# Performance work log

Measured on AMD Instinct MI355X. Metric: run time of the kernel, lower is better.

Reference implementation:

```python
import jax, jax.numpy as jnp
import numpy as np

SUBSET_CHANNELS = 128


def setup_inputs() -> dict:
    key = jax.random.key(0)
    k_in, k_q, k_k, k_v = jax.random.split(key, 4)
    B, S, C, D = 8, 2048, 1024, SUBSET_CHANNELS
    scale = 1.0 / np.sqrt(C)  # ~ default torch Linear init scale
    return {
        "input": jax.random.normal(k_in, (B, S, C), dtype=jnp.float32),
        "Wq": jax.random.normal(k_q, (C, D), dtype=jnp.float32) * scale,
        "Wk": jax.random.normal(k_k, (C, D), dtype=jnp.float32) * scale,
        "Wv": jax.random.normal(k_v, (C, D), dtype=jnp.float32) * scale,
    }


def reference(input, Wq, Wk, Wv):
    # Projections (bias=False): [B,S,C] @ [C,D] -> [B,S,D]
    Q = input @ Wq
    K = input @ Wk
    V = input @ Wv
    D = Wq.shape[1]
    # scores[b, i, j] = Q[b,i,:] . K[b,j,:], scaled by sqrt(subset_channels)
    scores = jnp.einsum("bqd,bkd->bqk", Q, K) / jnp.sqrt(jnp.asarray(D, Q.dtype))
    # NOTE: original applies softmax over dim=1 (the QUERY axis), non-standard.
    att = jax.nn.softmax(scores, axis=1)
    # output[b, i, :] = sum_j att[b,i,j] * V[b,j,:]
    return jnp.einsum("bqk,bkd->bqd", att, V)
```

## Files before the change

kernel.cpp:

```cpp
#include <hip/hip_runtime.h>
#include <hip/hip_bf16.h>

typedef __bf16 bf16_t;
typedef bf16_t bf16x4 __attribute__((ext_vector_type(4)));
typedef bf16_t bf16x8 __attribute__((ext_vector_type(8)));
typedef float f32x4 __attribute__((ext_vector_type(4)));
typedef __attribute__((address_space(1))) const unsigned int gu32_t;
typedef __attribute__((address_space(3))) unsigned int lu32_t;

#define MFMA(a, b, c) __builtin_amdgcn_mfma_f32_16x16x32_bf16(a, b, c, 0, 0, 0)

constexpr int B = 8, S = 2048, C = 1024, D = 128;
constexpr float C2 = 0.12751744f;


__global__ __launch_bounds__(256) void k_wt(const float* Wq, const float* Wk, const float* Wv, bf16_t* Wf) {
    int ct = blockIdx.x, w = blockIdx.y;
    const float* src = (w == 0) ? Wq : ((w == 1) ? Wk : Wv);
    __shared__ bf16_t tile[16][132];
    int t = threadIdx.x;
    int cr = t >> 4, dq = t & 15;
    const float* p = src + (size_t)(ct * 16 + cr) * D + dq * 8;
    f32x4 v0 = *(const f32x4*)p;
    f32x4 v1 = *(const f32x4*)(p + 4);
#pragma unroll
    for (int q = 0; q < 4; ++q) { tile[cr][dq * 8 + q] = (bf16_t)v0[q]; tile[cr][dq * 8 + 4 + q] = (bf16_t)v1[q]; }
    __syncthreads();
    int n = t >> 1, g = t & 1;
    bf16x8 o;
#pragma unroll
    for (int cc = 0; cc < 8; ++cc) o[cc] = tile[g * 8 + cc][n];
    int c8 = ct * 2 + g;
    int nblk = w * 8 + (n >> 4);
    size_t a = ((size_t)(nblk * 32 + (c8 >> 2)) * 64 + (c8 & 3) * 16 + (n & 15)) * 8;
    *(bf16x8*)(Wf + a) = o;
}

__global__ __launch_bounds__(512, 4) void k_qkv(const float* X, const bf16_t* Wf,
                                                bf16_t* Qf, bf16_t* Kf, float* Vf,
                                                float* Out) {
    __shared__ __align__(16) bf16_t xfr[64 * 512];
    int mt = blockIdx.x;
    int t = threadIdx.x;
    int lane = t & 63, wid = t >> 6;
    int lr = lane & 15, lg = lane >> 4;
    int rw = mt * 32;

    {
        f32x4* O4 = (f32x4*)Out;
        f32x4 z = {};
        int u = mt * 512 + t;
        O4[u] = z;
        O4[u + 262144] = z;
    }

    f32x4 xa[8], xb[8];
#pragma unroll
    for (int p = 0; p < 8; ++p) {
        int fi = p * 8 + wid;
        int m = rw + (fi >> 5) * 16 + lr;
        int c = (fi & 31) * 32 + lg * 8;
        const float* px = X + (size_t)m * C + c;
        xa[p] = *(const f32x4*)px;
        xb[p] = *(const f32x4*)(px + 4);
    }
#pragma unroll
    for (int p = 0; p < 8; ++p) {
        bf16x8 o;
#pragma unroll
        for (int q = 0; q < 4; ++q) { o[q] = (bf16_t)xa[p][q]; o[4 + q] = (bf16_t)xb[p][q]; }
        *(bf16x8*)&xfr[(size_t)(p * 8 + wid) * 512 + lane * 8] = o;
    }
    __syncthreads();

    f32x4 acc[2][3] = {};
    const bf16_t* wbase = Wf + (size_t)(wid * 3) * 32 * 512;
#pragma unroll 8
    for (int kk = 0; kk < 32; ++kk) {
        bf16x8 a0 = *(const bf16x8*)&xfr[(size_t)kk * 512 + lane * 8];
        bf16x8 a1 = *(const bf16x8*)&xfr[(size_t)(32 + kk) * 512 + lane * 8];
#pragma unroll
        for (int nf = 0; nf < 3; ++nf) {
            bf16x8 w = *(const bf16x8*)(wbase + ((size_t)(nf * 32 + kk)) * 512 + lane * 8);
            acc[0][nf] = MFMA(a0, w, acc[0][nf]);
            acc[1][nf] = MFMA(a1, w, acc[1][nf]);
        }
    }

#pragma unroll
    for (int mi = 0; mi < 2; ++mi)
#pragma unroll
        for (int nf = 0; nf < 3; ++nf) {
            int n = wid * 48 + nf * 16 + lr;
            int sel = (wid * 48 + nf * 16) >> 7;
            int nn = n & 127;
#pragma unroll
            for (int r = 0; r < 4; ++r) {
                int m = rw + mi * 16 + lg * 4 + r;
                float v = acc[mi][nf][r];
                if (sel == 2) {
                    Vf[(size_t)m * D + nn] = v;
                } else {
                    bf16_t* dst = (sel == 0) ? Qf : Kf;
                    size_t a = ((size_t)((m >> 4) * 4 + (nn >> 5)) * 64 + ((nn >> 3) & 3) * 16 + (m & 15)) * 8 + (nn & 7);
                    dst[a] = (bf16_t)v;
                }
            }
        }
}

__global__ __launch_bounds__(512, 4) void k_sum(const bf16_t* Qf, const bf16_t* Kf,
                                                const float* Vf, bf16_t* Vt2) {
    int l = blockIdx.x;
    int b = l & 7, jt = l >> 3;
    int j0 = jt * 32;
    int t = threadIdx.x;
    int lane = t & 63, wid = t >> 6;
    __shared__ __align__(16) bf16_t vtile[128 * 40];
    __shared__ float lsum[256];
    __shared__ float linv[32];

    bf16x8 kf[2][4];
    int jblkg = (b * S + j0) >> 4;
#pragma unroll
    for (int jF = 0; jF < 2; ++jF)
#pragma unroll
        for (int kk = 0; kk < 4; ++kk)
            kf[jF][kk] = *(const bf16x8*)(Kf + ((size_t)((jblkg + jF) * 4 + kk) * 64 + lane) * 8);

    float ls0 = 0.f, ls1 = 0.f;
#pragma unroll 4
    for (int tt = 0; tt < 16; ++tt) {
        int iblk = (b * S + wid * 256 + tt * 16) >> 4;
        bf16x8 qa[4];
#pragma unroll
        for (int kk = 0; kk < 4; ++kk)
            qa[kk] = *(const bf16x8*)(Qf + ((size_t)(iblk * 4 + kk) * 64 + lane) * 8);
        f32x4 s0 = {}, s1 = {};
#pragma unroll
        for (int kk = 0; kk < 4; ++kk) {
            s0 = MFMA(qa[kk], kf[0][kk], s0);
            s1 = MFMA(qa[kk], kf[1][kk], s1);
        }
#pragma unroll
        for (int r = 0; r < 4; ++r) { ls0 += exp2f(s0[r] * C2); ls1 += exp2f(s1[r] * C2); }
    }
    {
        float v0 = ls0 + __shfl_xor(ls0, 16); v0 += __shfl_xor(v0, 32);
        float v1 = ls1 + __shfl_xor(ls1, 16); v1 += __shfl_xor(v1, 32);
        if (lane < 16) { lsum[wid * 32 + lane] = v0; lsum[wid * 32 + 16 + lane] = v1; }
    }
    __syncthreads();
    if (t < 32) {
        float ss = 0.f;
#pragma unroll
        for (int w = 0; w < 8; ++w) ss += lsum[w * 32 + t];
        linv[t] = 1.0f / ss;
    }
    __syncthreads();
#pragma unroll
    for (int p = 0; p < 2; ++p) {
        int u = p * 512 + t;
        int jj = u & 31, dq = u >> 5;
        f32x4 v = *(const f32x4*)(Vf + (size_t)(b * S + j0 + jj) * D + dq * 4);
        float inv = linv[jj];
#pragma unroll
        for (int q = 0; q < 4; ++q)
            vtile[(dq * 4 + q) * 40 + jj] = (bf16_t)(v[q] * inv);
    }
    __syncthreads();
    {
        int d = t >> 2, jg = t & 3;
        bf16x8 row = *(const bf16x8*)&vtile[d * 40 + jg * 8];
        size_t j32g = (size_t)b * 64 + jt;
        size_t a = ((j32g * 8 + (d >> 4)) * 64 + jg * 16 + (d & 15)) * 8;
        *(bf16x8*)(Vt2 + a) = row;
    }
}

__global__ __launch_bounds__(512, 4) void k_out(const bf16_t* Qf, const bf16_t* Kf,
                                                const bf16_t* Vt2, float* Out) {
    int l = blockIdx.x;
    int b = l & 7, it = (l >> 3) & 31, jh = l >> 8;
    int ibase = it * 64;
    int t = threadIdx.x;
    int lane = t & 63, wid = t >> 6;
    int lr = lane & 15, lg = lane >> 4;
    int ig = wid >> 1, jq = wid & 1;
    __shared__ __align__(16) bf16_t pool[37888];
    bf16_t* klds = pool;
    bf16_t* vlds = pool + 16384;
    bf16_t* pl = pool + 32768 + wid * 640;

    bf16x8 qf[4];
    int iblk = (b * S + ibase + ig * 16) >> 4;
#pragma unroll
    for (int kk = 0; kk < 4; ++kk)
        qf[kk] = *(const bf16x8*)(Qf + ((size_t)(iblk * 4 + kk) * 64 + lane) * 8);

    f32x4 acc[8] = {};
    const bf16_t* kbase = Kf + (size_t)(b * S + jh * 1024) * 128 + wid * 1024 + lane * 8;
    const bf16_t* vbase = Vt2 + (size_t)(b * 64 + jh * 32) * 4096 + wid * 1024 + lane * 8;

    auto stageKV = [&](int bufi, int tt) {
        const bf16_t* gk = kbase + (size_t)tt * 8192;
        __builtin_amdgcn_global_load_lds((gu32_t*)gk, (lu32_t*)&klds[bufi * 8192 + wid * 1024], 16, 0, 0);
        __builtin_amdgcn_global_load_lds((gu32_t*)(gk + 512), (lu32_t*)&klds[bufi * 8192 + wid * 1024 + 512], 16, 0, 0);
        const bf16_t* gv = vbase + (size_t)tt * 8192;
        __builtin_amdgcn_global_load_lds((gu32_t*)gv, (lu32_t*)&vlds[bufi * 8192 + wid * 1024], 16, 0, 0);
        __builtin_amdgcn_global_load_lds((gu32_t*)(gv + 512), (lu32_t*)&vlds[bufi * 8192 + wid * 1024 + 512], 16, 0, 0);
    };
    stageKV(0, 0);
    __syncthreads();

    for (int tt = 0; tt < 16; ++tt) {
        int buf = tt & 1;
        if (tt < 15) stageKV(buf ^ 1, tt + 1);
#pragma unroll
        for (int jF = 0; jF < 2; ++jF) {
            const bf16_t* kl = &klds[buf * 8192 + ((jq * 2 + jF) * 4) * 512 + lane * 8];
            f32x4 s = {};
            s = MFMA(*(const bf16x8*)(kl), qf[0], s);
            s = MFMA(*(const bf16x8*)(kl + 512), qf[1], s);
            s = MFMA(*(const bf16x8*)(kl + 1024), qf[2], s);
            s = MFMA(*(const bf16x8*)(kl + 1536), qf[3], s);
            bf16x4 pv;
#pragma unroll
            for (int r = 0; r < 4; ++r) pv[r] = (bf16_t)exp2f(s[r] * C2);
            *(bf16x4*)&pl[lr * 40 + jF * 16 + lg * 4] = pv;
        }
        bf16x8 pa = *(const bf16x8*)&pl[lr * 40 + lg * 8];
        const bf16_t* vl = &vlds[buf * 8192 + jq * 4096 + lane * 8];
        __builtin_amdgcn_s_setprio(1);
#pragma unroll
        for (int dc = 0; dc < 8; ++dc)
            acc[dc] = MFMA(pa, *(const bf16x8*)(vl + dc * 512), acc[dc]);
        __builtin_amdgcn_s_setprio(0);
        __syncthreads();
    }

    float* R = (float*)pool + ig * 2048;
    if (jq == 1) {
#pragma unroll
        for (int dc = 0; dc < 8; ++dc)
#pragma unroll
            for (int r = 0; r < 4; ++r)
                R[(lg * 4 + r) * 128 + dc * 16 + lr] = acc[dc][r];
    }
    __syncthreads();
    if (jq == 0) {
#pragma unroll
        for (int dc = 0; dc < 8; ++dc)
#pragma unroll
            for (int r = 0; r < 4; ++r)
                atomicAdd(&Out[(size_t)(b * S + ibase + ig * 16 + lg * 4 + r) * 128 + dc * 16 + lr],
                          acc[dc][r] + R[(lg * 4 + r) * 128 + dc * 16 + lr]);
    }
}

extern "C" void kernel_launch(void* const* d_in, const int* in_sizes, int n_in,
                              void* d_out, int out_size, void* d_ws, size_t ws_size,
                              hipStream_t stream) {
    const float* X  = (const float*)d_in[0];
    const float* Wq = (const float*)d_in[1];
    const float* Wk = (const float*)d_in[2];
    const float* Wv = (const float*)d_in[3];
    char* ws = (char*)d_ws;
    bf16_t* Wf  = (bf16_t*)(ws);
    bf16_t* Qf  = (bf16_t*)(ws + (1ull << 20));
    bf16_t* Kf  = (bf16_t*)(ws + (5ull << 20));
    float*  Vf  = (float*)(ws + (9ull << 20));
    bf16_t* Vt2 = (bf16_t*)(ws + (17ull << 20));
    float* Out = (float*)d_out;

    k_wt<<<dim3(64, 3), dim3(256), 0, stream>>>(Wq, Wk, Wv, Wf);
    k_qkv<<<dim3(512), dim3(512), 0, stream>>>(X, Wf, Qf, Kf, Vf, Out);
    k_sum<<<dim3(512), dim3(512), 0, stream>>>(Qf, Kf, Vf, Vt2);
    k_out<<<dim3(512), dim3(512), 0, stream>>>(Qf, Kf, Vt2, Out);
}
```

Measured before the change: 87.37 us.

## Double row tiles in QKV projection and attention-output kernels, halving grid sizes

The projection kernel now handles 64 rows per block, staging X in two K-halves, so each weight fragment loaded from global memory is reused across four row fragments instead of two. The output kernel gives each wave its own 16 query rows over 128 rows per block instead of splitting the key range across wave pairs. This removes the LDS cross-wave reduction and shrinks the shared-memory footprint. Both grids drop to 256 blocks, which may underfill the GPU's compute units, and the output kernel now runs twice as many serial key/value tile iterations per block.

```diff
diff --git a/kernel.cpp b/kernel.cpp
--- a/kernel.cpp
+++ b/kernel.cpp
@@ -44,51 +44,61 @@
     int t = threadIdx.x;
     int lane = t & 63, wid = t >> 6;
     int lr = lane & 15, lg = lane >> 4;
-    int rw = mt * 32;
+    int rw = mt * 64;
 
     {
         f32x4* O4 = (f32x4*)Out;
         f32x4 z = {};
         int u = mt * 512 + t;
-        O4[u] = z;
-        O4[u + 262144] = z;
-    }
-
-    f32x4 xa[8], xb[8];
-#pragma unroll
-    for (int p = 0; p < 8; ++p) {
-        int fi = p * 8 + wid;
-        int m = rw + (fi >> 5) * 16 + lr;
-        int c = (fi & 31) * 32 + lg * 8;
-        const float* px = X + (size_t)m * C + c;
-        xa[p] = *(const f32x4*)px;
-        xb[p] = *(const f32x4*)(px + 4);
-    }
-#pragma unroll
-    for (int p = 0; p < 8; ++p) {
-        bf16x8 o;
-#pragma unroll
-        for (int q = 0; q < 4; ++q) { o[q] = (bf16_t)xa[p][q]; o[4 + q] = (bf16_t)xb[p][q]; }
-        *(bf16x8*)&xfr[(size_t)(p * 8 + wid) * 512 + lane * 8] = o;
-    }
-    __syncthreads();
-
-    f32x4 acc[2][3] = {};
-    const bf16_t* wbase = Wf + (size_t)(wid * 3) * 32 * 512;
-#pragma unroll 8
-    for (int kk = 0; kk < 32; ++kk) {
-        bf16x8 a0 = *(const bf16x8*)&xfr[(size_t)kk * 512 + lane * 8];
-        bf16x8 a1 = *(const bf16x8*)&xfr[(size_t)(32 + kk) * 512 + lane * 8];
-#pragma unroll
-        for (int nf = 0; nf < 3; ++nf) {
-            bf16x8 w = *(const bf16x8*)(wbase + ((size_t)(nf * 32 + kk)) * 512 + lane * 8);
-            acc[0][nf] = MFMA(a0, w, acc[0][nf]);
-            acc[1][nf] = MFMA(a1, w, acc[1][nf]);
-        }
-    }
-
-#pragma unroll
-    for (int mi = 0; mi < 2; ++mi)
+        O4[u] = z; O4[u + 131072] = z; O4[u + 262144] = z; O4[u + 393216] = z;
+    }
+
+    auto stage = [&](int h) {
+        f32x4 xa[8], xb[8];
+#pragma unroll
+        for (int p = 0; p < 8; ++p) {
+            int fi = p * 8 + wid;
+            int m = rw + (fi >> 4) * 16 + lr;
+            int c = h * 512 + (fi & 15) * 32 + lg * 8;
+            const float* px = X + (size_t)m * C + c;
+            xa[p] = *(const f32x4*)px;
+            xb[p] = *(const f32x4*)(px + 4);
+        }
+#pragma unroll
+        for (int p = 0; p < 8; ++p) {
+            bf16x8 o;
+#pragma unroll
+            for (int q = 0; q < 4; ++q) { o[q] = (bf16_t)xa[p][q]; o[4 + q] = (bf16_t)xb[p][q]; }
+            *(bf16x8*)&xfr[(size_t)(p * 8 + wid) * 512 + lane * 8] = o;
+        }
+    };
+
+    f32x4 acc[4][3] = {};
+    const bf16_t* wbase = Wf + (size_t)(wid * 3) * 32 * 512 + lane * 8;
+
+    stage(0);
+    __syncthreads();
+#pragma unroll
+    for (int h = 0; h < 2; ++h) {
+        if (h) { __syncthreads(); stage(1); __syncthreads(); }
+#pragma unroll 4
+        for (int kk = 0; kk < 16; ++kk) {
+            int kkg = h * 16 + kk;
+            bf16x8 w[3];
+#pragma unroll
+            for (int nf = 0; nf < 3; ++nf)
+                w[nf] = *(const bf16x8*)(wbase + (size_t)(nf * 32 + kkg) * 512);
+#pragma unroll
+            for (int rF = 0; rF < 4; ++rF) {
+                bf16x8 a = *(const bf16x8*)&xfr[(size_t)(rF * 16 + kk) * 512 + lane * 8];
+                acc[rF][0] = MFMA(a, w[0], acc[rF][0]);
+                acc[rF][1] = MFMA(a, w[1], acc[rF][1]);
+                acc[rF][2] = MFMA(a, w[2], acc[rF][2]);
+            }
+        }
+    }
+#pragma unroll
+    for (int rF = 0; rF < 4; ++rF)
 #pragma unroll
         for (int nf = 0; nf < 3; ++nf) {
             int n = wid * 48 + nf * 16 + lr;
@@ -96,8 +106,8 @@
             int nn = n & 127;
 #pragma unroll
             for (int r = 0; r < 4; ++r) {
-                int m = rw + mi * 16 + lg * 4 + r;
-                float v = acc[mi][nf][r];
+                int m = rw + rF * 16 + lg * 4 + r;
+                float v = acc[rF][nf][r];
                 if (sel == 2) {
                     Vf[(size_t)m * D + nn] = v;
                 } else {
@@ -181,44 +191,41 @@
 __global__ __launch_bounds__(512, 4) void k_out(const bf16_t* Qf, const bf16_t* Kf,
                                                 const bf16_t* Vt2, float* Out) {
     int l = blockIdx.x;
-    int b = l & 7, it = (l >> 3) & 31, jh = l >> 8;
-    int ibase = it * 64;
+    int b = l & 7, it = (l >> 3) & 15, jh = l >> 7;
+    int ibase = it * 128;
     int t = threadIdx.x;
     int lane = t & 63, wid = t >> 6;
     int lr = lane & 15, lg = lane >> 4;
-    int ig = wid >> 1, jq = wid & 1;
-    __shared__ __align__(16) bf16_t pool[37888];
+    __shared__ __align__(16) bf16_t pool[21504];
     bf16_t* klds = pool;
-    bf16_t* vlds = pool + 16384;
-    bf16_t* pl = pool + 32768 + wid * 640;
+    bf16_t* vlds = pool + 8192;
+    bf16_t* pl = pool + 16384 + wid * 640;
 
     bf16x8 qf[4];
-    int iblk = (b * S + ibase + ig * 16) >> 4;
+    int iblk = (b * S + ibase + wid * 16) >> 4;
 #pragma unroll
     for (int kk = 0; kk < 4; ++kk)
         qf[kk] = *(const bf16x8*)(Qf + ((size_t)(iblk * 4 + kk) * 64 + lane) * 8);
 
     f32x4 acc[8] = {};
-    const bf16_t* kbase = Kf + (size_t)(b * S + jh * 1024) * 128 + wid * 1024 + lane * 8;
-    const bf16_t* vbase = Vt2 + (size_t)(b * 64 + jh * 32) * 4096 + wid * 1024 + lane * 8;
+    const bf16_t* kbase = Kf + ((size_t)((b * S + jh * 1024) >> 4)) * 2048 + t * 8;
+    const bf16_t* vbase = Vt2 + (size_t)(b * 64 + jh * 32) * 4096 + t * 8;
 
     auto stageKV = [&](int bufi, int tt) {
-        const bf16_t* gk = kbase + (size_t)tt * 8192;
-        __builtin_amdgcn_global_load_lds((gu32_t*)gk, (lu32_t*)&klds[bufi * 8192 + wid * 1024], 16, 0, 0);
-        __builtin_amdgcn_global_load_lds((gu32_t*)(gk + 512), (lu32_t*)&klds[bufi * 8192 + wid * 1024 + 512], 16, 0, 0);
-        const bf16_t* gv = vbase + (size_t)tt * 8192;
-        __builtin_amdgcn_global_load_lds((gu32_t*)gv, (lu32_t*)&vlds[bufi * 8192 + wid * 1024], 16, 0, 0);
-        __builtin_amdgcn_global_load_lds((gu32_t*)(gv + 512), (lu32_t*)&vlds[bufi * 8192 + wid * 1024 + 512], 16, 0, 0);
+        __builtin_amdgcn_global_load_lds((gu32_t*)(kbase + (size_t)tt * 4096),
+                                         (lu32_t*)&klds[bufi * 4096 + t * 8], 16, 0, 0);
+        __builtin_amdgcn_global_load_lds((gu32_t*)(vbase + (size_t)tt * 4096),
+                                         (lu32_t*)&vlds[bufi * 4096 + t * 8], 16, 0, 0);
     };
     stageKV(0, 0);
     __syncthreads();
 
-    for (int tt = 0; tt < 16; ++tt) {
+    for (int tt = 0; tt < 32; ++tt) {
         int buf = tt & 1;
-        if (tt < 15) stageKV(buf ^ 1, tt + 1);
+        if (tt < 31) stageKV(buf ^ 1, tt + 1);
 #pragma unroll
         for (int jF = 0; jF < 2; ++jF) {
-            const bf16_t* kl = &klds[buf * 8192 + ((jq * 2 + jF) * 4) * 512 + lane * 8];
+            const bf16_t* kl = &klds[buf * 4096 + jF * 2048 + lane * 8];
             f32x4 s = {};
             s = MFMA(*(const bf16x8*)(kl), qf[0], s);
             s = MFMA(*(const bf16x8*)(kl + 512), qf[1], s);
@@ -230,7 +237,7 @@
             *(bf16x4*)&pl[lr * 40 + jF * 16 + lg * 4] = pv;
         }
         bf16x8 pa = *(const bf16x8*)&pl[lr * 40 + lg * 8];
-        const bf16_t* vl = &vlds[buf * 8192 + jq * 4096 + lane * 8];
+        const bf16_t* vl = &vlds[buf * 4096 + lane * 8];
         __builtin_amdgcn_s_setprio(1);
 #pragma unroll
         for (int dc = 0; dc < 8; ++dc)
@@ -239,23 +246,12 @@
         __syncthreads();
     }
 
-    float* R = (float*)pool + ig * 2048;
-    if (jq == 1) {
-#pragma unroll
-        for (int dc = 0; dc < 8; ++dc)
-#pragma unroll
-            for (int r = 0; r < 4; ++r)
-                R[(lg * 4 + r) * 128 + dc * 16 + lr] = acc[dc][r];
-    }
-    __syncthreads();
-    if (jq == 0) {
-#pragma unroll
-        for (int dc = 0; dc < 8; ++dc)
-#pragma unroll
-            for (int r = 0; r < 4; ++r)
-                atomicAdd(&Out[(size_t)(b * S + ibase + ig * 16 + lg * 4 + r) * 128 + dc * 16 + lr],
-                          acc[dc][r] + R[(lg * 4 + r) * 128 + dc * 16 + lr]);
-    }
+#pragma unroll
+    for (int dc = 0; dc < 8; ++dc)
+#pragma unroll
+        for (int r = 0; r < 4; ++r)
+            atomicAdd(&Out[(size_t)(b * S + ibase + wid * 16 + lg * 4 + r) * 128 + dc * 16 + lr],
+                      acc[dc][r]);
 }
 
 extern "C" void kernel_launch(void* const* d_in, const int* in_sizes, int n_in,
@@ -274,7 +270,7 @@
     float* Out = (float*)d_out;
 
     k_wt<<<dim3(64, 3), dim3(256), 0, stream>>>(Wq, Wk, Wv, Wf);
-    k_qkv<<<dim3(512), dim3(512), 0, stream>>>(X, Wf, Qf, Kf, Vf, Out);
+    k_qkv<<<dim3(256), dim3(512), 0, stream>>>(X, Wf, Qf, Kf, Vf, Out);
     k_sum<<<dim3(512), dim3(512), 0, stream>>>(Qf, Kf, Vf, Vt2);
-    k_out<<<dim3(512), dim3(512), 0, stream>>>(Qf, Kf, Vt2, Out);
-}
+    k_out<<<dim3(256), dim3(512), 0, stream>>>(Qf, Kf, Vt2, Out);
+}
```

New measurement: 94.08 us. 1.08x slower.

## Enlarge QKV projection tile to 64 rows with staged K halves and LDS epilogue

Applied to the files above, without the earlier changes.

The QKV projection kernel now handles 64 rows per block (256 blocks instead of 512), so each weight fragment loaded from global memory feeds four MFMA row tiles instead of two. The X tile is staged into LDS in two K-halves so shared memory stays bounded. Weight fragments are double-buffered in registers one k-step ahead. Outputs are staged through LDS and written out as coalesced vector stores instead of scattered scalar stores. The cost is fewer blocks (less parallelism across CUs), more accumulator registers, and extra barriers between the halves.

```diff
diff --git a/kernel.cpp b/kernel.cpp
--- a/kernel.cpp
+++ b/kernel.cpp
@@ -39,74 +39,122 @@
 __global__ __launch_bounds__(512, 4) void k_qkv(const float* X, const bf16_t* Wf,
                                                 bf16_t* Qf, bf16_t* Kf, float* Vf,
                                                 float* Out) {
-    __shared__ __align__(16) bf16_t xfr[64 * 512];
+    __shared__ __align__(16) char pool_[67072];
+    bf16_t* xfr = (bf16_t*)pool_;
+    bf16_t* qkL = (bf16_t*)pool_;
+    float*  vL  = (float*)(pool_ + 33792);
     int mt = blockIdx.x;
     int t = threadIdx.x;
     int lane = t & 63, wid = t >> 6;
     int lr = lane & 15, lg = lane >> 4;
-    int rw = mt * 32;
+    int rw = mt * 64;
 
     {
         f32x4* O4 = (f32x4*)Out;
         f32x4 z = {};
         int u = mt * 512 + t;
-        O4[u] = z;
-        O4[u + 262144] = z;
-    }
-
-    f32x4 xa[8], xb[8];
-#pragma unroll
-    for (int p = 0; p < 8; ++p) {
-        int fi = p * 8 + wid;
-        int m = rw + (fi >> 5) * 16 + lr;
-        int c = (fi & 31) * 32 + lg * 8;
-        const float* px = X + (size_t)m * C + c;
-        xa[p] = *(const f32x4*)px;
-        xb[p] = *(const f32x4*)(px + 4);
-    }
-#pragma unroll
-    for (int p = 0; p < 8; ++p) {
-        bf16x8 o;
-#pragma unroll
-        for (int q = 0; q < 4; ++q) { o[q] = (bf16_t)xa[p][q]; o[4 + q] = (bf16_t)xb[p][q]; }
-        *(bf16x8*)&xfr[(size_t)(p * 8 + wid) * 512 + lane * 8] = o;
-    }
-    __syncthreads();
-
-    f32x4 acc[2][3] = {};
-    const bf16_t* wbase = Wf + (size_t)(wid * 3) * 32 * 512;
-#pragma unroll 8
-    for (int kk = 0; kk < 32; ++kk) {
-        bf16x8 a0 = *(const bf16x8*)&xfr[(size_t)kk * 512 + lane * 8];
-        bf16x8 a1 = *(const bf16x8*)&xfr[(size_t)(32 + kk) * 512 + lane * 8];
-#pragma unroll
-        for (int nf = 0; nf < 3; ++nf) {
-            bf16x8 w = *(const bf16x8*)(wbase + ((size_t)(nf * 32 + kk)) * 512 + lane * 8);
-            acc[0][nf] = MFMA(a0, w, acc[0][nf]);
-            acc[1][nf] = MFMA(a1, w, acc[1][nf]);
-        }
-    }
-
-#pragma unroll
-    for (int mi = 0; mi < 2; ++mi)
+        O4[u] = z; O4[u + 131072] = z; O4[u + 262144] = z; O4[u + 393216] = z;
+    }
+
+    auto stage = [&](int h) {
+#pragma unroll
+        for (int pp = 0; pp < 2; ++pp) {
+            f32x4 xa[4], xb[4];
+#pragma unroll
+            for (int p = 0; p < 4; ++p) {
+                int fi = (pp * 4 + p) * 8 + wid;
+                int m = rw + (fi >> 4) * 16 + lr;
+                int c = h * 512 + (fi & 15) * 32 + lg * 8;
+                const float* px = X + (size_t)m * C + c;
+                xa[p] = *(const f32x4*)px;
+                xb[p] = *(const f32x4*)(px + 4);
+            }
+#pragma unroll
+            for (int p = 0; p < 4; ++p) {
+                bf16x8 o;
+#pragma unroll
+                for (int q = 0; q < 4; ++q) { o[q] = (bf16_t)xa[p][q]; o[4 + q] = (bf16_t)xb[p][q]; }
+                *(bf16x8*)&xfr[(size_t)((pp * 4 + p) * 8 + wid) * 512 + lane * 8] = o;
+            }
+        }
+    };
+
+    f32x4 acc[4][3] = {};
+    const bf16_t* wbase = Wf + (size_t)(wid * 3) * 32 * 512 + lane * 8;
+    auto wld = [&](int nf, int kkg) {
+        return *(const bf16x8*)(wbase + (size_t)(nf * 32 + kkg) * 512);
+    };
+
+    stage(0);
+    bf16x8 wb0[3], wb1[3];
+#pragma unroll
+    for (int nf = 0; nf < 3; ++nf) wb0[nf] = wld(nf, 0);
+    __syncthreads();
+
+#pragma unroll
+    for (int h = 0; h < 2; ++h) {
+        if (h) { __syncthreads(); stage(1); __syncthreads(); }
+#pragma unroll
+        for (int kk = 0; kk < 16; ++kk) {
+            int kkg = h * 16 + kk;
+            bool even = ((kkg & 1) == 0);
+            if (kkg < 31) {
+#pragma unroll
+                for (int nf = 0; nf < 3; ++nf) {
+                    if (even) wb1[nf] = wld(nf, kkg + 1);
+                    else      wb0[nf] = wld(nf, kkg + 1);
+                }
+            }
+#pragma unroll
+            for (int rF = 0; rF < 4; ++rF) {
+                bf16x8 a = *(const bf16x8*)&xfr[(size_t)(rF * 16 + kk) * 512 + lane * 8];
+                if (even) {
+                    acc[rF][0] = MFMA(a, wb0[0], acc[rF][0]);
+                    acc[rF][1] = MFMA(a, wb0[1], acc[rF][1]);
+                    acc[rF][2] = MFMA(a, wb0[2], acc[rF][2]);
+                } else {
+                    acc[rF][0] = MFMA(a, wb1[0], acc[rF][0]);
+                    acc[rF][1] = MFMA(a, wb1[1], acc[rF][1]);
+                    acc[rF][2] = MFMA(a, wb1[2], acc[rF][2]);
+                }
+            }
+        }
+    }
+
+    __syncthreads();
+#pragma unroll
+    for (int rF = 0; rF < 4; ++rF)
 #pragma unroll
         for (int nf = 0; nf < 3; ++nf) {
             int n = wid * 48 + nf * 16 + lr;
             int sel = (wid * 48 + nf * 16) >> 7;
-            int nn = n & 127;
 #pragma unroll
             for (int r = 0; r < 4; ++r) {
-                int m = rw + mi * 16 + lg * 4 + r;
-                float v = acc[mi][nf][r];
-                if (sel == 2) {
-                    Vf[(size_t)m * D + nn] = v;
-                } else {
-                    bf16_t* dst = (sel == 0) ? Qf : Kf;
-                    size_t a = ((size_t)((m >> 4) * 4 + (nn >> 5)) * 64 + ((nn >> 3) & 3) * 16 + (m & 15)) * 8 + (nn & 7);
-                    dst[a] = (bf16_t)v;
-                }
-            }
-        }
+                int mloc = rF * 16 + lg * 4 + r;
+                float v = acc[rF][nf][r];
+                if (sel == 2) vL[mloc * 132 + (n - 256)] = v;
+                else          qkL[mloc * 264 + n] = (bf16_t)v;
+            }
+        }
+    __syncthreads();
+#pragma unroll
+    for (int p = 0; p < 4; ++p) {
+        int F = wid * 4 + p;
+        int isK = F >> 4, iblk = F & 3, dblk = (F >> 2) & 3;
+        int m16 = lane & 15, kg = lane >> 4;
+        int col = isK * 128 + dblk * 32 + kg * 8;
+        bf16x8 o = *(const bf16x8*)&qkL[(iblk * 16 + m16) * 264 + col];
+        bf16_t* dst = isK ? Kf : Qf;
+        size_t frg = (size_t)((rw >> 4) + iblk) * 4 + dblk;
+        *(bf16x8*)(dst + (frg * 64 + lane) * 8) = o;
+    }
+#pragma unroll
+    for (int p = 0; p < 4; ++p) {
+        int u = p * 512 + t;
+        int m = u >> 5, dq = u & 31;
+        f32x4 v = *(const f32x4*)&vL[m * 132 + dq * 4];
+        *(f32x4*)(Vf + (size_t)(rw + m) * D + dq * 4) = v;
+    }
 }
 
 __global__ __launch_bounds__(512, 4) void k_sum(const bf16_t* Qf, const bf16_t* Kf,
@@ -274,7 +322,7 @@
     float* Out = (float*)d_out;
 
     k_wt<<<dim3(64, 3), dim3(256), 0, stream>>>(Wq, Wk, Wv, Wf);
-    k_qkv<<<dim3(512), dim3(512), 0, stream>>>(X, Wf, Qf, Kf, Vf, Out);
+    k_qkv<<<dim3(256), dim3(512), 0, stream>>>(X, Wf, Qf, Kf, Vf, Out);
     k_sum<<<dim3(512), dim3(512), 0, stream>>>(Qf, Kf, Vf, Vt2);
     k_out<<<dim3(512), dim3(512), 0, stream>>>(Qf, Kf, Vt2, Out);
 }
```

After: 87.14 us. Within noise of the previous version (-0.3%).

## Prefetch weight fragments in registers and stage QKV outputs through LDS

Applied to the files above, without the earlier changes.

The QKV projection kernel now preloads weight fragments three k-steps ahead in a rotating register buffer, fully unrolls the k loop, and raises wave priority around the MFMA groups. The weight loads are issued before the barrier so their latency overlaps the X-to-LDS conversion. Output scatter of single bf16/float elements is replaced by staging results in LDS and writing vectorized fragments. Nontemporal loads and stores are used for X, the zeroed Out buffer and Q/K/V. The trade-off is higher register pressure from the prefetch buffers and an extra barrier.

```diff
diff --git a/kernel.cpp b/kernel.cpp
--- a/kernel.cpp
+++ b/kernel.cpp
@@ -39,7 +39,10 @@
 __global__ __launch_bounds__(512, 4) void k_qkv(const float* X, const bf16_t* Wf,
                                                 bf16_t* Qf, bf16_t* Kf, float* Vf,
                                                 float* Out) {
-    __shared__ __align__(16) bf16_t xfr[64 * 512];
+    __shared__ __align__(16) char pool_[65536];
+    bf16_t* xfr = (bf16_t*)pool_;
+    bf16_t* qkL = (bf16_t*)pool_;
+    float*  vL  = (float*)(pool_ + 16896);
     int mt = blockIdx.x;
     int t = threadIdx.x;
     int lane = t & 63, wid = t >> 6;
@@ -50,63 +53,96 @@
         f32x4* O4 = (f32x4*)Out;
         f32x4 z = {};
         int u = mt * 512 + t;
-        O4[u] = z;
-        O4[u + 262144] = z;
-    }
-
-    f32x4 xa[8], xb[8];
-#pragma unroll
-    for (int p = 0; p < 8; ++p) {
-        int fi = p * 8 + wid;
-        int m = rw + (fi >> 5) * 16 + lr;
-        int c = (fi & 31) * 32 + lg * 8;
-        const float* px = X + (size_t)m * C + c;
-        xa[p] = *(const f32x4*)px;
-        xb[p] = *(const f32x4*)(px + 4);
-    }
-#pragma unroll
-    for (int p = 0; p < 8; ++p) {
-        bf16x8 o;
-#pragma unroll
-        for (int q = 0; q < 4; ++q) { o[q] = (bf16_t)xa[p][q]; o[4 + q] = (bf16_t)xb[p][q]; }
-        *(bf16x8*)&xfr[(size_t)(p * 8 + wid) * 512 + lane * 8] = o;
-    }
-    __syncthreads();
+        __builtin_nontemporal_store(z, O4 + u);
+        __builtin_nontemporal_store(z, O4 + u + 262144);
+    }
+
+    {
+        f32x4 xa[8], xb[8];
+#pragma unroll
+        for (int p = 0; p < 8; ++p) {
+            int fi = p * 8 + wid;
+            int m = rw + (fi >> 5) * 16 + lr;
+            int c = (fi & 31) * 32 + lg * 8;
+            const f32x4* px = (const f32x4*)(X + (size_t)m * C + c);
+            xa[p] = __builtin_nontemporal_load(px);
+            xb[p] = __builtin_nontemporal_load(px + 1);
+        }
+#pragma unroll
+        for (int p = 0; p < 8; ++p) {
+            bf16x8 o;
+#pragma unroll
+            for (int q = 0; q < 4; ++q) { o[q] = (bf16_t)xa[p][q]; o[4 + q] = (bf16_t)xb[p][q]; }
+            *(bf16x8*)&xfr[(size_t)(p * 8 + wid) * 512 + lane * 8] = o;
+        }
+    }
 
     f32x4 acc[2][3] = {};
-    const bf16_t* wbase = Wf + (size_t)(wid * 3) * 32 * 512;
-#pragma unroll 8
+    const bf16_t* wbase = Wf + (size_t)(wid * 3) * 32 * 512 + lane * 8;
+    auto wld = [&](int nf, int kkg) {
+        return *(const bf16x8*)(wbase + (size_t)(nf * 32 + kkg) * 512);
+    };
+
+    bf16x8 wr_[3][3];
+#pragma unroll
+    for (int d = 0; d < 3; ++d)
+#pragma unroll
+        for (int nf = 0; nf < 3; ++nf) wr_[d][nf] = wld(nf, d);
+    __syncthreads();
+
+#pragma unroll
     for (int kk = 0; kk < 32; ++kk) {
+        int slot = kk % 3;
         bf16x8 a0 = *(const bf16x8*)&xfr[(size_t)kk * 512 + lane * 8];
         bf16x8 a1 = *(const bf16x8*)&xfr[(size_t)(32 + kk) * 512 + lane * 8];
-#pragma unroll
-        for (int nf = 0; nf < 3; ++nf) {
-            bf16x8 w = *(const bf16x8*)(wbase + ((size_t)(nf * 32 + kk)) * 512 + lane * 8);
-            acc[0][nf] = MFMA(a0, w, acc[0][nf]);
-            acc[1][nf] = MFMA(a1, w, acc[1][nf]);
-        }
-    }
-
+        __builtin_amdgcn_s_setprio(1);
+        acc[0][0] = MFMA(a0, wr_[slot][0], acc[0][0]);
+        acc[1][0] = MFMA(a1, wr_[slot][0], acc[1][0]);
+        acc[0][1] = MFMA(a0, wr_[slot][1], acc[0][1]);
+        acc[1][1] = MFMA(a1, wr_[slot][1], acc[1][1]);
+        acc[0][2] = MFMA(a0, wr_[slot][2], acc[0][2]);
+        acc[1][2] = MFMA(a1, wr_[slot][2], acc[1][2]);
+        __builtin_amdgcn_s_setprio(0);
+        if (kk < 29) {
+#pragma unroll
+            for (int nf = 0; nf < 3; ++nf) wr_[slot][nf] = wld(nf, kk + 3);
+        }
+    }
+
+    __syncthreads();
 #pragma unroll
     for (int mi = 0; mi < 2; ++mi)
 #pragma unroll
         for (int nf = 0; nf < 3; ++nf) {
             int n = wid * 48 + nf * 16 + lr;
             int sel = (wid * 48 + nf * 16) >> 7;
-            int nn = n & 127;
 #pragma unroll
             for (int r = 0; r < 4; ++r) {
-                int m = rw + mi * 16 + lg * 4 + r;
+                int mloc = mi * 16 + lg * 4 + r;
                 float v = acc[mi][nf][r];
-                if (sel == 2) {
-                    Vf[(size_t)m * D + nn] = v;
-                } else {
-                    bf16_t* dst = (sel == 0) ? Qf : Kf;
-                    size_t a = ((size_t)((m >> 4) * 4 + (nn >> 5)) * 64 + ((nn >> 3) & 3) * 16 + (m & 15)) * 8 + (nn & 7);
-                    dst[a] = (bf16_t)v;
-                }
+                if (sel == 2) vL[mloc * 132 + (n - 256)] = v;
+                else          qkL[mloc * 264 + n] = (bf16_t)v;
             }
         }
+    __syncthreads();
+#pragma unroll
+    for (int p = 0; p < 2; ++p) {
+        int F = wid * 2 + p;
+        int isK = F >> 3, iblk = (F >> 2) & 1, dblk = F & 3;
+        int m16 = lane & 15, kg = lane >> 4;
+        int col = isK * 128 + dblk * 32 + kg * 8;
+        bf16x8 o = *(const bf16x8*)&qkL[(iblk * 16 + m16) * 264 + col];
+        bf16_t* dst = isK ? Kf : Qf;
+        size_t frg = (size_t)((rw >> 4) + iblk) * 4 + dblk;
+        __builtin_nontemporal_store(o, (bf16x8*)(dst + (frg * 64 + lane) * 8));
+    }
+#pragma unroll
+    for (int p = 0; p < 2; ++p) {
+        int u = p * 512 + t;
+        int m = u >> 5, dq = u & 31;
+        f32x4 v = *(const f32x4*)&vL[m * 132 + dq * 4];
+        __builtin_nontemporal_store(v, (f32x4*)(Vf + (size_t)(rw + m) * D + dq * 4));
+    }
 }
 
 __global__ __launch_bounds__(512, 4) void k_sum(const bf16_t* Qf, const bf16_t* Kf,
```

After: 95.29 us. 1.09x slower.
